# Optimization experiments

Hardware: AMD Instinct MI355X
Metric: run time of the kernel (lower is better)

Reference implementation:

```python
import jax, jax.numpy as jnp
import numpy as np

B, S, D = 2, 2048, 512
E, K = 8, 2
H = 4 * D  # expert_dim
EPS = 1e-10


def setup_inputs() -> dict:
    key = jax.random.key(0)
    ks = jax.random.split(key, 5)
    scale = 1.0 / np.sqrt(D)
    return {
        "x": jax.random.normal(ks[0], (B, S, D), dtype=jnp.float32),
        "w_router": jax.random.normal(ks[1], (D, E), dtype=jnp.float32) * scale,
        "w_gate": jax.random.normal(ks[2], (D, E * H), dtype=jnp.float32) * scale,
        "w_up": jax.random.normal(ks[3], (D, E * H), dtype=jnp.float32) * scale,
        "w_down": jax.random.normal(ks[4], (H, D), dtype=jnp.float32) * (1.0 / np.sqrt(H)),
    }


def reference(x, w_router, w_gate, w_up, w_down):
    b, s, d = x.shape
    n = b * s
    xf = x.reshape(n, d)

    # Router: softmax over experts, pick top-k, renormalize
    router_probs = jax.nn.softmax(xf @ w_router, axis=-1)          # [N, E]
    top_p, top_i = jax.lax.top_k(router_probs, K)                  # [N, K]
    top_p = top_p / (top_p.sum(axis=-1, keepdims=True) + EPS)

    # Dense all-expert gate/up projections (as in original module)
    gate = jax.nn.silu(xf @ w_gate).reshape(n, E, H)               # [N, E, H]
    up = (xf @ w_up).reshape(n, E, H)                              # [N, E, H]

    # Gather per-token top-k expert slices and combine
    sel_gate = jnp.take_along_axis(gate, top_i[:, :, None], axis=1)  # [N, K, H]
    sel_up = jnp.take_along_axis(up, top_i[:, :, None], axis=1)      # [N, K, H]
    combined = jnp.sum(top_p[:, :, None] * sel_gate * sel_up, axis=1)  # [N, H]

    out = (combined @ w_down).reshape(b, s, d)

    # Load-balancing aux loss
    expert_probs = router_probs.mean(axis=0)                       # [E]
    lb_loss = E * jnp.sum(expert_probs * jnp.log(expert_probs * E + EPS))
    return out, lb_loss
```

## Files before the change

kernel.cpp:

```cpp
#include <hip/hip_runtime.h>
#include <hip/hip_bf16.h>

#define N_TOK 4096
#define D_DIM 512
#define E_NUM 8
#define H_DIM 2048

typedef __attribute__((ext_vector_type(8))) short short8;
typedef __attribute__((ext_vector_type(4))) float f32x4;

__device__ inline short f2bs(float f) {
  __hip_bfloat16 h = __float2bfloat16(f);
  return *reinterpret_cast<short*>(&h);
}

__device__ inline void llds16(const short* g, short* l) {
  __builtin_amdgcn_global_load_lds(
      (const __attribute__((address_space(1))) void*)g,
      (__attribute__((address_space(3))) void*)l, 16, 0, 0);
}

__global__ void __launch_bounds__(256) prep_kernel(
    const float* __restrict__ wg, const float* __restrict__ wu,
    const float* __restrict__ wd, short* __restrict__ wgb,
    short* __restrict__ wub, short* __restrict__ wdb,
    int* __restrict__ e_cnt, float* __restrict__ loss_acc,
    int* __restrict__ loss_cnt) {
  int u = blockIdx.x;
  int tid = threadIdx.x;
  if (u < 17408) {
    __shared__ float tbuf[32][33];
    const float* in;
    short* op;
    int R, C, c0, r0;
    if (u < 16384) {
      in = (u < 8192) ? wg : wu;
      op = (u < 8192) ? wgb : wub;
      int v = u & 8191;
      R = D_DIM; C = E_NUM * H_DIM;
      c0 = (v & 511) * 32; r0 = (v >> 9) * 32;
    } else {
      in = wd; op = wdb;
      int v = u - 16384;
      R = H_DIM; C = D_DIM;
      c0 = (v & 15) * 32; r0 = (v >> 4) * 32;
    }
    int tx = tid & 31, ty = tid >> 5;
#pragma unroll
    for (int i = 0; i < 4; ++i)
      tbuf[ty + 8 * i][tx] = in[(size_t)(r0 + ty + 8 * i) * C + c0 + tx];
    __syncthreads();
#pragma unroll
    for (int i = 0; i < 4; ++i)
      op[(size_t)(c0 + ty + 8 * i) * R + r0 + tx] = f2bs(tbuf[tx][ty + 8 * i]);
  } else {
    if (tid < 8) { e_cnt[tid] = 0; loss_acc[tid] = 0.f; }
    if (tid == 8) *loss_cnt = 0;
  }
}

__global__ void __launch_bounds__(256) router_kernel(
    const float* __restrict__ x, const float* __restrict__ wr,
    short* __restrict__ xb, int* __restrict__ e_cnt,
    int* __restrict__ e_tok, float* __restrict__ e_p,
    float* __restrict__ loss_acc, int* __restrict__ loss_cnt,
    float* __restrict__ out_loss) {
  __shared__ float wr_lds[D_DIM * 9];
  __shared__ int h_cnt[E_NUM];
  __shared__ int h_base[E_NUM];
  __shared__ float psum[E_NUM];
  int tid = threadIdx.x;

  for (int i = tid; i < D_DIM * E_NUM; i += 256)
    wr_lds[(i >> 3) * 9 + (i & 7)] = wr[i];
  if (tid < E_NUM) { h_cnt[tid] = 0; psum[tid] = 0.f; }
  __syncthreads();

  int r = tid >> 3, pp = tid & 7;
  int t = blockIdx.x * 32 + r;
  const float* xr0 = x + (size_t)t * D_DIM;
  short* xw0 = xb + (size_t)t * D_DIM;
  float acc[8] = {0, 0, 0, 0, 0, 0, 0, 0};
#pragma unroll 4
  for (int j = 0; j < 16; ++j) {
    int d = j * 32 + pp * 4;
    float4 xv = *(const float4*)(xr0 + d);
    short4 o;
    o.x = f2bs(xv.x); o.y = f2bs(xv.y); o.z = f2bs(xv.z); o.w = f2bs(xv.w);
    *(short4*)(xw0 + d) = o;
    const float* w = &wr_lds[d * 9];
#pragma unroll
    for (int e = 0; e < 8; ++e)
      acc[e] += xv.x * w[e] + xv.y * w[9 + e] + xv.z * w[18 + e] + xv.w * w[27 + e];
  }
#pragma unroll
  for (int e = 0; e < 8; ++e) {
    acc[e] += __shfl_xor(acc[e], 1);
    acc[e] += __shfl_xor(acc[e], 2);
    acc[e] += __shfl_xor(acc[e], 4);
  }

  bool leader = (pp == 0);
  int i0 = 0, i1 = 1, l0 = 0, l1 = 0;
  float q0 = 0.f, q1 = 0.f;
  if (leader) {
    float m = acc[0];
#pragma unroll
    for (int e = 1; e < 8; ++e) m = fmaxf(m, acc[e]);
    float p[8], s = 0.f;
#pragma unroll
    for (int e = 0; e < 8; ++e) { p[e] = expf(acc[e] - m); s += p[e]; }
    float inv = 1.f / s;
#pragma unroll
    for (int e = 0; e < 8; ++e) {
      p[e] *= inv;
      atomicAdd(&psum[e], p[e]);
    }
    i0 = 0;
#pragma unroll
    for (int e = 1; e < 8; ++e) if (p[e] > p[i0]) i0 = e;
    i1 = (i0 == 0) ? 1 : 0;
#pragma unroll
    for (int e = 0; e < 8; ++e) if (e != i0 && p[e] > p[i1]) i1 = e;
    float ps = p[i0] + p[i1] + 1e-10f;
    q0 = p[i0] / ps; q1 = p[i1] / ps;
    l0 = atomicAdd(&h_cnt[i0], 1);
    l1 = atomicAdd(&h_cnt[i1], 1);
  }
  __syncthreads();
  if (tid < E_NUM) {
    h_base[tid] = h_cnt[tid] ? atomicAdd(&e_cnt[tid], h_cnt[tid]) : 0;
    atomicAdd(&loss_acc[tid], psum[tid]);
  }
  __syncthreads();
  if (leader) {
    int s0 = h_base[i0] + l0;
    e_tok[i0 * N_TOK + s0] = t * 2 + 0; e_p[i0 * N_TOK + s0] = q0;
    int s1 = h_base[i1] + l1;
    e_tok[i1 * N_TOK + s1] = t * 2 + 1; e_p[i1 * N_TOK + s1] = q1;
  }
  __threadfence();
  __syncthreads();
  if (tid == 0) {
    int c = atomicAdd(loss_cnt, 1);
    if (c == 127) {
      float lb = 0.f;
#pragma unroll
      for (int e = 0; e < 8; ++e) {
        float pe = atomicAdd(&loss_acc[e], 0.f) / (float)N_TOK;
        lb += pe * logf(pe * 8.f + 1e-10f);
      }
      out_loss[0] = 8.f * lb;
    }
  }
}

__global__ void __launch_bounds__(256, 2) moe_gateup_kernel(
    const short* __restrict__ xb, const short* __restrict__ wg,
    const short* __restrict__ wu, const int* __restrict__ e_cnt,
    const int* __restrict__ e_tok, const float* __restrict__ e_p,
    short* __restrict__ act) {
  __shared__ __align__(16) short As[256 * 64];
  __shared__ __align__(16) short Bgs[64 * 64];
  __shared__ __align__(16) short Bus[64 * 64];
  __shared__ int s_row[256];
  __shared__ float s_pr[256];

  int e = blockIdx.z;
  int n_e = e_cnt[e];
  int rt = blockIdx.y;
  if (rt * 256 >= n_e) return;
  int h0 = blockIdx.x * 64;
  int tid = threadIdx.x;
  int lane = tid & 63, wid = tid >> 6;

  {
    int r = rt * 256 + tid;
    bool v = r < n_e;
    s_row[tid] = v ? e_tok[e * N_TOK + r] : -1;
    s_pr[tid] = v ? e_p[e * N_TOK + r] : 0.f;
  }
  __syncthreads();

  int cg = (lane & 7) ^ (lane >> 3);
  const short* baseA[8];
  const short* baseB[4];
  short* ldsA = As + (size_t)wid * 64 * 64;
  short* ldsB;
#pragma unroll
  for (int jj = 0; jj < 8; ++jj) {
    int r = wid * 64 + jj * 8 + (lane >> 3);
    int row = s_row[r];
    int t = (row < 0) ? 0 : (row >> 1);
    baseA[jj] = xb + (size_t)t * D_DIM + cg * 8;
  }
  {
    const short* wB = ((wid & 2) ? wu : wg) + (size_t)e * H_DIM * D_DIM;
    int rb = (wid & 1) * 32;
    ldsB = ((wid & 2) ? Bus : Bgs) + rb * 64;
#pragma unroll
    for (int jj = 0; jj < 4; ++jj) {
      int h = h0 + rb + jj * 8 + (lane >> 3);
      baseB[jj] = wB + (size_t)h * D_DIM + cg * 8;
    }
  }

  int ml = lane & 15, quad = lane >> 4;
  int m0w = wid * 64;
  f32x4 accG[4][4], accU[4][4];
#pragma unroll
  for (int mf = 0; mf < 4; ++mf)
#pragma unroll
    for (int nf = 0; nf < 4; ++nf) {
      accG[mf][nf] = (f32x4){0, 0, 0, 0};
      accU[mf][nf] = (f32x4){0, 0, 0, 0};
    }

  for (int kt = 0; kt < D_DIM / 64; ++kt) {
    int kb = kt * 64;
#pragma unroll
    for (int jj = 0; jj < 8; ++jj)
      llds16(baseA[jj] + kb, ldsA + jj * 8 * 64);
#pragma unroll
    for (int jj = 0; jj < 4; ++jj)
      llds16(baseB[jj] + kb, ldsB + jj * 8 * 64);
    __syncthreads();
#pragma unroll
    for (int ks = 0; ks < 2; ++ks) {
      int cs = ((quad + ks * 4) ^ (ml & 7)) * 8;
      short8 a[4], bg[4], bu[4];
#pragma unroll
      for (int mf = 0; mf < 4; ++mf)
        a[mf] = *(const short8*)&As[(m0w + mf * 16 + ml) * 64 + cs];
#pragma unroll
      for (int nf = 0; nf < 4; ++nf) {
        bg[nf] = *(const short8*)&Bgs[(nf * 16 + ml) * 64 + cs];
        bu[nf] = *(const short8*)&Bus[(nf * 16 + ml) * 64 + cs];
      }
#pragma unroll
      for (int mf = 0; mf < 4; ++mf)
#pragma unroll
        for (int nf = 0; nf < 4; ++nf) {
          accG[mf][nf] = __builtin_amdgcn_mfma_f32_16x16x32_bf16(a[mf], bg[nf], accG[mf][nf], 0, 0, 0);
          accU[mf][nf] = __builtin_amdgcn_mfma_f32_16x16x32_bf16(a[mf], bu[nf], accU[mf][nf], 0, 0, 0);
        }
    }
    __syncthreads();
  }

#pragma unroll
  for (int mf = 0; mf < 4; ++mf)
#pragma unroll
    for (int r = 0; r < 4; ++r) {
      int rl = m0w + mf * 16 + quad * 4 + r;
      int arow = s_row[rl];
      if (arow >= 0) {
        float pr = s_pr[rl];
#pragma unroll
        for (int nf = 0; nf < 4; ++nf) {
          float g = accG[mf][nf][r], u = accU[mf][nf][r];
          float val = pr * (g / (1.f + __expf(-g))) * u;
          act[(size_t)arow * H_DIM + h0 + nf * 16 + ml] = f2bs(val);
        }
      }
    }
}

__global__ void __launch_bounds__(256, 3) down_kernel(
    const short* __restrict__ act, const short* __restrict__ wd,
    float* __restrict__ partial) {
  __shared__ __align__(16) short As[128 * 64];
  __shared__ __align__(16) short Bs[128 * 64];
  int d0 = blockIdx.x * 128;
  int t0 = blockIdx.y * 128;
  int ksb = blockIdx.z;
  int tid = threadIdx.x, lane = tid & 63, wid = tid >> 6;
  int cg = (lane & 7) ^ (lane >> 3);

  const short* baseA[4];
  const short* baseB[4];
  short* ldsA = As + (size_t)wid * 32 * 64;
  short* ldsB = Bs + (size_t)wid * 32 * 64;
#pragma unroll
  for (int jj = 0; jj < 4; ++jj) {
    int r = wid * 32 + jj * 8 + (lane >> 3);
    baseA[jj] = act + (size_t)(2 * (t0 + r)) * H_DIM + cg * 8;
    int d = d0 + wid * 32 + jj * 8 + (lane >> 3);
    baseB[jj] = wd + (size_t)d * H_DIM + cg * 8;
  }

  int ml = lane & 15, quad = lane >> 4;
  int m0w = (wid & 1) * 64, n0w = (wid >> 1) * 64;
  f32x4 acc[4][4];
#pragma unroll
  for (int mf = 0; mf < 4; ++mf)
#pragma unroll
    for (int nf = 0; nf < 4; ++nf) acc[mf][nf] = (f32x4){0, 0, 0, 0};

  for (int kt = ksb * 16; kt < ksb * 16 + 16; ++kt) {
    size_t offA = (size_t)(kt & 1) * H_DIM + (kt >> 1) * 64;
    int offB = (kt >> 1) * 64;
#pragma unroll
    for (int jj = 0; jj < 4; ++jj) {
      llds16(baseA[jj] + offA, ldsA + jj * 8 * 64);
      llds16(baseB[jj] + offB, ldsB + jj * 8 * 64);
    }
    __syncthreads();
#pragma unroll
    for (int ks = 0; ks < 2; ++ks) {
      int cs = ((quad + ks * 4) ^ (ml & 7)) * 8;
      short8 a[4], b[4];
#pragma unroll
      for (int mf = 0; mf < 4; ++mf)
        a[mf] = *(const short8*)&As[(m0w + mf * 16 + ml) * 64 + cs];
#pragma unroll
      for (int nf = 0; nf < 4; ++nf)
        b[nf] = *(const short8*)&Bs[(n0w + nf * 16 + ml) * 64 + cs];
#pragma unroll
      for (int mf = 0; mf < 4; ++mf)
#pragma unroll
        for (int nf = 0; nf < 4; ++nf)
          acc[mf][nf] = __builtin_amdgcn_mfma_f32_16x16x32_bf16(a[mf], b[nf], acc[mf][nf], 0, 0, 0);
    }
    __syncthreads();
  }

  float* pout = partial + (size_t)ksb * N_TOK * D_DIM;
#pragma unroll
  for (int mf = 0; mf < 4; ++mf)
#pragma unroll
    for (int r = 0; r < 4; ++r) {
      int t = t0 + m0w + mf * 16 + quad * 4 + r;
#pragma unroll
      for (int nf = 0; nf < 4; ++nf)
        pout[(size_t)t * D_DIM + d0 + n0w + nf * 16 + ml] = acc[mf][nf][r];
    }
}

__global__ void __launch_bounds__(256) reduce_kernel(
    const float* __restrict__ partial, float* __restrict__ out) {
  int i = blockIdx.x * 256 + threadIdx.x;
  const int Q = N_TOK * D_DIM / 4;
  const float4* p = (const float4*)partial;
  float4 a = p[i], b = p[i + Q], c = p[i + 2 * Q], d = p[i + 3 * Q];
  float4 r = {a.x + b.x + c.x + d.x, a.y + b.y + c.y + d.y,
              a.z + b.z + c.z + d.z, a.w + b.w + c.w + d.w};
  ((float4*)out)[i] = r;
}

extern "C" void kernel_launch(void* const* d_in, const int* in_sizes, int n_in,
                              void* d_out, int out_size, void* d_ws, size_t ws_size,
                              hipStream_t stream) {
  const float* x = (const float*)d_in[0];
  const float* wr = (const float*)d_in[1];
  const float* wg = (const float*)d_in[2];
  const float* wu = (const float*)d_in[3];
  const float* wd = (const float*)d_in[4];
  float* out = (float*)d_out;

  char* ws = (char*)d_ws;
  size_t off = 0;
  auto alloc = [&](size_t bytes) {
    char* p = ws + off;
    off += (bytes + 255) & ~(size_t)255;
    return p;
  };
  short* xb = (short*)alloc((size_t)N_TOK * D_DIM * 2);
  short* wgb = (short*)alloc((size_t)E_NUM * H_DIM * D_DIM * 2);
  short* wub = (short*)alloc((size_t)E_NUM * H_DIM * D_DIM * 2);
  short* wdb = (short*)alloc((size_t)D_DIM * H_DIM * 2);
  short* act = (short*)alloc((size_t)N_TOK * 2 * H_DIM * 2);
  float* partial = (float*)alloc((size_t)4 * N_TOK * D_DIM * 4);
  int* e_cnt = (int*)alloc(256);
  int* e_tok = (int*)alloc((size_t)E_NUM * N_TOK * 4);
  float* e_p = (float*)alloc((size_t)E_NUM * N_TOK * 4);
  float* loss_acc = (float*)alloc(256);
  int* loss_cnt = (int*)alloc(256);

  prep_kernel<<<17409, 256, 0, stream>>>(wg, wu, wd, wgb, wub, wdb,
                                         e_cnt, loss_acc, loss_cnt);
  router_kernel<<<N_TOK / 32, 256, 0, stream>>>(x, wr, xb, e_cnt, e_tok, e_p,
                                                loss_acc, loss_cnt,
                                                out + (size_t)N_TOK * D_DIM);
  moe_gateup_kernel<<<dim3(H_DIM / 64, N_TOK / 256, E_NUM), 256, 0, stream>>>(
      xb, wgb, wub, e_cnt, e_tok, e_p, act);
  down_kernel<<<dim3(D_DIM / 128, N_TOK / 128, 4), 256, 0, stream>>>(act, wdb, partial);
  reduce_kernel<<<N_TOK * D_DIM / 4 / 256, 256, 0, stream>>>(partial, out);
}
```

Before: 242.3 us.

## Fuse router into weight-prep kernel and replace global atomics with per-block buckets

Merges the router into the weight conversion launch as extra blocks, removing one kernel launch. The global atomic expert counters and the last-block loss finalisation are replaced by per-block bucket counts. The gate/up kernel now rebuilds expert row lists with an LDS prefix scan plus binary search, and an extra z-slice computes the load-balancing loss. This removes the serial dependency and the atomics, at the cost of a 256-entry scan in every gate/up block.

```diff
diff --git a/kernel.cpp b/kernel.cpp
--- a/kernel.cpp
+++ b/kernel.cpp
@@ -5,6 +5,7 @@
 #define D_DIM 512
 #define E_NUM 8
 #define H_DIM 2048
+#define RB_NUM 256
 
 typedef __attribute__((ext_vector_type(8))) short short8;
 typedef __attribute__((ext_vector_type(4))) float f32x4;
@@ -20,30 +21,33 @@
       (__attribute__((address_space(3))) void*)l, 16, 0, 0);
 }
 
-__global__ void __launch_bounds__(256) prep_kernel(
+__global__ void __launch_bounds__(256) prep_router_kernel(
     const float* __restrict__ wg, const float* __restrict__ wu,
-    const float* __restrict__ wd, short* __restrict__ wgb,
-    short* __restrict__ wub, short* __restrict__ wdb,
-    int* __restrict__ e_cnt, float* __restrict__ loss_acc,
-    int* __restrict__ loss_cnt) {
+    const float* __restrict__ wd, const float* __restrict__ x,
+    const float* __restrict__ wr, short* __restrict__ wgb,
+    short* __restrict__ wub, short* __restrict__ wdb, short* __restrict__ xb,
+    int* __restrict__ cnt_blk, int* __restrict__ tok_bkt,
+    float* __restrict__ p_bkt, float* __restrict__ psum_blk) {
   int u = blockIdx.x;
   int tid = threadIdx.x;
-  if (u < 17408) {
+
+  if (u >= RB_NUM) {
     __shared__ float tbuf[32][33];
+    int v = u - RB_NUM;
     const float* in;
     short* op;
     int R, C, c0, r0;
-    if (u < 16384) {
-      in = (u < 8192) ? wg : wu;
-      op = (u < 8192) ? wgb : wub;
-      int v = u & 8191;
+    if (v < 16384) {
+      in = (v < 8192) ? wg : wu;
+      op = (v < 8192) ? wgb : wub;
+      int w = v & 8191;
       R = D_DIM; C = E_NUM * H_DIM;
-      c0 = (v & 511) * 32; r0 = (v >> 9) * 32;
+      c0 = (w & 511) * 32; r0 = (w >> 9) * 32;
     } else {
       in = wd; op = wdb;
-      int v = u - 16384;
+      int w = v - 16384;
       R = H_DIM; C = D_DIM;
-      c0 = (v & 15) * 32; r0 = (v >> 4) * 32;
+      c0 = (w & 15) * 32; r0 = (w >> 4) * 32;
     }
     int tx = tid & 31, ty = tid >> 5;
 #pragma unroll
@@ -53,57 +57,45 @@
 #pragma unroll
     for (int i = 0; i < 4; ++i)
       op[(size_t)(c0 + ty + 8 * i) * R + r0 + tx] = f2bs(tbuf[tx][ty + 8 * i]);
-  } else {
-    if (tid < 8) { e_cnt[tid] = 0; loss_acc[tid] = 0.f; }
-    if (tid == 8) *loss_cnt = 0;
-  }
-}
-
-__global__ void __launch_bounds__(256) router_kernel(
-    const float* __restrict__ x, const float* __restrict__ wr,
-    short* __restrict__ xb, int* __restrict__ e_cnt,
-    int* __restrict__ e_tok, float* __restrict__ e_p,
-    float* __restrict__ loss_acc, int* __restrict__ loss_cnt,
-    float* __restrict__ out_loss) {
-  __shared__ float wr_lds[D_DIM * 9];
+    return;
+  }
+
+  __shared__ float wr_t[E_NUM * D_DIM];
   __shared__ int h_cnt[E_NUM];
-  __shared__ int h_base[E_NUM];
-  __shared__ float psum[E_NUM];
-  int tid = threadIdx.x;
-
+  __shared__ float psh[E_NUM];
+  int rb = u;
   for (int i = tid; i < D_DIM * E_NUM; i += 256)
-    wr_lds[(i >> 3) * 9 + (i & 7)] = wr[i];
-  if (tid < E_NUM) { h_cnt[tid] = 0; psum[tid] = 0.f; }
+    wr_t[(i & 7) * D_DIM + (i >> 3)] = wr[i];
+  if (tid < E_NUM) { h_cnt[tid] = 0; psh[tid] = 0.f; }
   __syncthreads();
 
-  int r = tid >> 3, pp = tid & 7;
-  int t = blockIdx.x * 32 + r;
+  int r = tid >> 4, pp = tid & 15;
+  int t = rb * 16 + r;
   const float* xr0 = x + (size_t)t * D_DIM;
   short* xw0 = xb + (size_t)t * D_DIM;
   float acc[8] = {0, 0, 0, 0, 0, 0, 0, 0};
-#pragma unroll 4
-  for (int j = 0; j < 16; ++j) {
-    int d = j * 32 + pp * 4;
+#pragma unroll
+  for (int j = 0; j < 8; ++j) {
+    int d = j * 64 + pp * 4;
     float4 xv = *(const float4*)(xr0 + d);
     short4 o;
     o.x = f2bs(xv.x); o.y = f2bs(xv.y); o.z = f2bs(xv.z); o.w = f2bs(xv.w);
     *(short4*)(xw0 + d) = o;
-    const float* w = &wr_lds[d * 9];
-#pragma unroll
-    for (int e = 0; e < 8; ++e)
-      acc[e] += xv.x * w[e] + xv.y * w[9 + e] + xv.z * w[18 + e] + xv.w * w[27 + e];
+#pragma unroll
+    for (int e = 0; e < 8; ++e) {
+      float4 w = *(const float4*)&wr_t[e * D_DIM + d];
+      acc[e] += xv.x * w.x + xv.y * w.y + xv.z * w.z + xv.w * w.w;
+    }
   }
 #pragma unroll
   for (int e = 0; e < 8; ++e) {
     acc[e] += __shfl_xor(acc[e], 1);
     acc[e] += __shfl_xor(acc[e], 2);
     acc[e] += __shfl_xor(acc[e], 4);
-  }
-
-  bool leader = (pp == 0);
-  int i0 = 0, i1 = 1, l0 = 0, l1 = 0;
-  float q0 = 0.f, q1 = 0.f;
-  if (leader) {
+    acc[e] += __shfl_xor(acc[e], 8);
+  }
+
+  if (pp == 0) {
     float m = acc[0];
 #pragma unroll
     for (int e = 1; e < 8; ++e) m = fmaxf(m, acc[e]);
@@ -114,74 +106,98 @@
 #pragma unroll
     for (int e = 0; e < 8; ++e) {
       p[e] *= inv;
-      atomicAdd(&psum[e], p[e]);
-    }
-    i0 = 0;
+      atomicAdd(&psh[e], p[e]);
+    }
+    int i0 = 0;
 #pragma unroll
     for (int e = 1; e < 8; ++e) if (p[e] > p[i0]) i0 = e;
-    i1 = (i0 == 0) ? 1 : 0;
+    int i1 = (i0 == 0) ? 1 : 0;
 #pragma unroll
     for (int e = 0; e < 8; ++e) if (e != i0 && p[e] > p[i1]) i1 = e;
     float ps = p[i0] + p[i1] + 1e-10f;
-    q0 = p[i0] / ps; q1 = p[i1] / ps;
-    l0 = atomicAdd(&h_cnt[i0], 1);
-    l1 = atomicAdd(&h_cnt[i1], 1);
+    float q0 = p[i0] / ps, q1 = p[i1] / ps;
+    int l0 = atomicAdd(&h_cnt[i0], 1);
+    int l1 = atomicAdd(&h_cnt[i1], 1);
+    tok_bkt[i0 * (RB_NUM * 16) + rb * 16 + l0] = t * 2 + 0;
+    p_bkt[i0 * (RB_NUM * 16) + rb * 16 + l0] = q0;
+    tok_bkt[i1 * (RB_NUM * 16) + rb * 16 + l1] = t * 2 + 1;
+    p_bkt[i1 * (RB_NUM * 16) + rb * 16 + l1] = q1;
   }
   __syncthreads();
   if (tid < E_NUM) {
-    h_base[tid] = h_cnt[tid] ? atomicAdd(&e_cnt[tid], h_cnt[tid]) : 0;
-    atomicAdd(&loss_acc[tid], psum[tid]);
-  }
-  __syncthreads();
-  if (leader) {
-    int s0 = h_base[i0] + l0;
-    e_tok[i0 * N_TOK + s0] = t * 2 + 0; e_p[i0 * N_TOK + s0] = q0;
-    int s1 = h_base[i1] + l1;
-    e_tok[i1 * N_TOK + s1] = t * 2 + 1; e_p[i1 * N_TOK + s1] = q1;
-  }
-  __threadfence();
-  __syncthreads();
-  if (tid == 0) {
-    int c = atomicAdd(loss_cnt, 1);
-    if (c == 127) {
+    cnt_blk[rb * 8 + tid] = h_cnt[tid];
+    psum_blk[rb * 8 + tid] = psh[tid];
+  }
+}
+
+__global__ void __launch_bounds__(256, 2) moe_gateup_kernel(
+    const short* __restrict__ xb, const short* __restrict__ wg,
+    const short* __restrict__ wu, const int* __restrict__ cnt_blk,
+    const int* __restrict__ tok_bkt, const float* __restrict__ p_bkt,
+    const float* __restrict__ psum_blk, short* __restrict__ act,
+    float* __restrict__ out_loss) {
+  int e = blockIdx.z;
+  int tid = threadIdx.x;
+
+  if (e == 8) {
+    if (blockIdx.x || blockIdx.y) return;
+    __shared__ float sums[8];
+    if (tid < 8) sums[tid] = 0.f;
+    __syncthreads();
+#pragma unroll
+    for (int ee = 0; ee < 8; ++ee)
+      atomicAdd(&sums[ee], psum_blk[tid * 8 + ee]);
+    __syncthreads();
+    if (tid == 0) {
       float lb = 0.f;
 #pragma unroll
-      for (int e = 0; e < 8; ++e) {
-        float pe = atomicAdd(&loss_acc[e], 0.f) / (float)N_TOK;
+      for (int ee = 0; ee < 8; ++ee) {
+        float pe = sums[ee] / (float)N_TOK;
         lb += pe * logf(pe * 8.f + 1e-10f);
       }
       out_loss[0] = 8.f * lb;
     }
-  }
-}
-
-__global__ void __launch_bounds__(256, 2) moe_gateup_kernel(
-    const short* __restrict__ xb, const short* __restrict__ wg,
-    const short* __restrict__ wu, const int* __restrict__ e_cnt,
-    const int* __restrict__ e_tok, const float* __restrict__ e_p,
-    short* __restrict__ act) {
+    return;
+  }
+
   __shared__ __align__(16) short As[256 * 64];
   __shared__ __align__(16) short Bgs[64 * 64];
   __shared__ __align__(16) short Bus[64 * 64];
+  __shared__ int scan[256];
   __shared__ int s_row[256];
   __shared__ float s_pr[256];
 
-  int e = blockIdx.z;
-  int n_e = e_cnt[e];
+  scan[tid] = cnt_blk[tid * 8 + e];
+  __syncthreads();
+  for (int ofs = 1; ofs < 256; ofs <<= 1) {
+    int v = (tid >= ofs) ? scan[tid - ofs] : 0;
+    __syncthreads();
+    scan[tid] += v;
+    __syncthreads();
+  }
+  int n_e = scan[255];
   int rt = blockIdx.y;
   if (rt * 256 >= n_e) return;
   int h0 = blockIdx.x * 64;
-  int tid = threadIdx.x;
-  int lane = tid & 63, wid = tid >> 6;
 
   {
     int r = rt * 256 + tid;
-    bool v = r < n_e;
-    s_row[tid] = v ? e_tok[e * N_TOK + r] : -1;
-    s_pr[tid] = v ? e_p[e * N_TOK + r] : 0.f;
+    int srow = -1;
+    float spr = 0.f;
+    if (r < n_e) {
+      int lo = 0, hi = 255;
+      while (lo < hi) { int mid = (lo + hi) >> 1; if (scan[mid] > r) hi = mid; else lo = mid + 1; }
+      int prev = lo ? scan[lo - 1] : 0;
+      int idx = e * (RB_NUM * 16) + lo * 16 + (r - prev);
+      srow = tok_bkt[idx];
+      spr = p_bkt[idx];
+    }
+    s_row[tid] = srow;
+    s_pr[tid] = spr;
   }
   __syncthreads();
 
+  int lane = tid & 63, wid = tid >> 6;
   int cg = (lane & 7) ^ (lane >> 3);
   const short* baseA[8];
   const short* baseB[4];
@@ -371,19 +387,16 @@
   short* wdb = (short*)alloc((size_t)D_DIM * H_DIM * 2);
   short* act = (short*)alloc((size_t)N_TOK * 2 * H_DIM * 2);
   float* partial = (float*)alloc((size_t)4 * N_TOK * D_DIM * 4);
-  int* e_cnt = (int*)alloc(256);
-  int* e_tok = (int*)alloc((size_t)E_NUM * N_TOK * 4);
-  float* e_p = (float*)alloc((size_t)E_NUM * N_TOK * 4);
-  float* loss_acc = (float*)alloc(256);
-  int* loss_cnt = (int*)alloc(256);
-
-  prep_kernel<<<17409, 256, 0, stream>>>(wg, wu, wd, wgb, wub, wdb,
-                                         e_cnt, loss_acc, loss_cnt);
-  router_kernel<<<N_TOK / 32, 256, 0, stream>>>(x, wr, xb, e_cnt, e_tok, e_p,
-                                                loss_acc, loss_cnt,
-                                                out + (size_t)N_TOK * D_DIM);
-  moe_gateup_kernel<<<dim3(H_DIM / 64, N_TOK / 256, E_NUM), 256, 0, stream>>>(
-      xb, wgb, wub, e_cnt, e_tok, e_p, act);
+  int* cnt_blk = (int*)alloc((size_t)RB_NUM * E_NUM * 4);
+  int* tok_bkt = (int*)alloc((size_t)E_NUM * RB_NUM * 16 * 4);
+  float* p_bkt = (float*)alloc((size_t)E_NUM * RB_NUM * 16 * 4);
+  float* psum_blk = (float*)alloc((size_t)RB_NUM * E_NUM * 4);
+
+  prep_router_kernel<<<RB_NUM + 17408, 256, 0, stream>>>(
+      wg, wu, wd, x, wr, wgb, wub, wdb, xb, cnt_blk, tok_bkt, p_bkt, psum_blk);
+  moe_gateup_kernel<<<dim3(H_DIM / 64, N_TOK / 256, E_NUM + 1), 256, 0, stream>>>(
+      xb, wgb, wub, cnt_blk, tok_bkt, p_bkt, psum_blk, act,
+      out + (size_t)N_TOK * D_DIM);
   down_kernel<<<dim3(D_DIM / 128, N_TOK / 128, 4), 256, 0, stream>>>(act, wdb, partial);
   reduce_kernel<<<N_TOK * D_DIM / 4 / 256, 256, 0, stream>>>(partial, out);
 }
```

After: 215.9 us. -10.9%, faster.
